# Performance work log

Measured on AMD Instinct MI355X. Metric: run time of the kernel, lower is better.

## Reference

```python
import jax, jax.numpy as jnp
import numpy as np

N_SETS = [5, 5, 5, 5, 5]
N_SAMPLES = 16384


def _rule_indices(n_sets):
    # (R, n) grid of all fuzzy-set index combinations, same as torch.meshgrid(indexing='ij')
    grids = np.meshgrid(*[np.arange(s) for s in n_sets], indexing='ij')
    return np.stack([g.reshape(-1) for g in grids], axis=1)  # (R, n)


def setup_inputs() -> dict:
    key = jax.random.key(0)
    ks = jax.random.split(key, len(N_SETS))
    return {
        f"m{j}": jax.random.uniform(ks[j], (N_SAMPLES, N_SETS[j]), dtype=jnp.float32)
        for j in range(len(N_SETS))
    }


def reference(m0, m1, m2, m3, m4):
    memberships = [m0, m1, m2, m3, m4]
    ri = jnp.asarray(_rule_indices(N_SETS))  # (R, n) static rule-index table
    # Gather per-variable membership columns for every rule and AND (prod) across variables.
    # Equivalent to padding/stacking + gather + prod over the variable axis in the original,
    # but avoids materializing the (n, N, R) int index tensor.
    ant = memberships[0][:, ri[:, 0]]  # (N, R)
    for j in range(1, len(N_SETS)):
        ant = ant * memberships[j][:, ri[:, j]]
    return ant  # (N, R)
```

## Files before the change

kernel.cpp:

```cpp
#include <hip/hip_runtime.h>


#define NSAMP 16384
#define NRULE 3125

__global__ __launch_bounds__(256) void antecedents_kernel(
    const float* __restrict__ m0, const float* __restrict__ m1,
    const float* __restrict__ m2, const float* __restrict__ m3,
    const float* __restrict__ m4, float* __restrict__ out)
{
    __shared__ float p012[125];
    __shared__ float p34[25];

    const int i = blockIdx.x;
    const unsigned t = threadIdx.x;

    if (t < 125u) {
        const unsigned a = t / 25u;
        const unsigned b = (t / 5u) % 5u;
        const unsigned c = t % 5u;
        p012[t] = m0[i * 5 + a] * m1[i * 5 + b] * m2[i * 5 + c];
    } else if (t < 150u) {
        const unsigned u = t - 125u;
        const unsigned d = u / 5u;
        const unsigned e = u % 5u;
        p34[u] = m3[i * 5 + d] * m4[i * 5 + e];
    }
    __syncthreads();

    float* __restrict__ orow = out + (size_t)i * NRULE;
    for (unsigned r = t; r < NRULE; r += 256u) {
        const unsigned hi = r / 25u;
        const unsigned lo = r - hi * 25u;
        orow[r] = p012[hi] * p34[lo];
    }
}

extern "C" void kernel_launch(void* const* d_in, const int* in_sizes, int n_in,
                              void* d_out, int out_size, void* d_ws, size_t ws_size,
                              hipStream_t stream) {
    const float* m0 = (const float*)d_in[0];
    const float* m1 = (const float*)d_in[1];
    const float* m2 = (const float*)d_in[2];
    const float* m3 = (const float*)d_in[3];
    const float* m4 = (const float*)d_in[4];
    float* out = (float*)d_out;

    antecedents_kernel<<<NSAMP, 256, 0, stream>>>(m0, m1, m2, m3, m4, out);
}
```

Before: 38.08 us.

## Process eight rows per block and write output with float4 stores

Each block now handles eight sample rows, building their partial-product tables together in shared memory. It writes the contiguous eight-row output chunk with 16-byte vector stores. This is meant to cut per-block launch and sync overhead and to use wider, fully aligned stores, since eight rows of 3125 floats is a multiple of four. The cost is more index arithmetic per element, including divisions by NRULE and 25, and fewer blocks in the grid.

Result: slower. 39.45 us (+3.6%).

```diff
diff --git a/kernel.cpp b/kernel.cpp
--- a/kernel.cpp
+++ b/kernel.cpp
@@ -3,36 +3,54 @@
 
 #define NSAMP 16384
 #define NRULE 3125
+#define ROWS_PER_BLOCK 8
+#define CHUNK_ELEMS (ROWS_PER_BLOCK * NRULE)
+#define CHUNK_VEC4 (CHUNK_ELEMS / 4)
 
 __global__ __launch_bounds__(256) void antecedents_kernel(
     const float* __restrict__ m0, const float* __restrict__ m1,
     const float* __restrict__ m2, const float* __restrict__ m3,
     const float* __restrict__ m4, float* __restrict__ out)
 {
-    __shared__ float p012[125];
-    __shared__ float p34[25];
+    __shared__ float p012[ROWS_PER_BLOCK][125];
+    __shared__ float p34[ROWS_PER_BLOCK][25];
 
-    const int i = blockIdx.x;
     const unsigned t = threadIdx.x;
+    const unsigned row0 = blockIdx.x * ROWS_PER_BLOCK;
 
-    if (t < 125u) {
-        const unsigned a = t / 25u;
-        const unsigned b = (t / 5u) % 5u;
-        const unsigned c = t % 5u;
-        p012[t] = m0[i * 5 + a] * m1[i * 5 + b] * m2[i * 5 + c];
-    } else if (t < 150u) {
-        const unsigned u = t - 125u;
-        const unsigned d = u / 5u;
-        const unsigned e = u % 5u;
-        p34[u] = m3[i * 5 + d] * m4[i * 5 + e];
+    for (unsigned u = t; u < ROWS_PER_BLOCK * 150u; u += 256u) {
+        const unsigned rr = u / 150u;
+        const unsigned k = u - rr * 150u;
+        const unsigned row = row0 + rr;
+        if (k < 125u) {
+            const unsigned a = k / 25u;
+            const unsigned b = (k / 5u) % 5u;
+            const unsigned c = k % 5u;
+            p012[rr][k] = m0[row * 5 + a] * m1[row * 5 + b] * m2[row * 5 + c];
+        } else {
+            const unsigned kk = k - 125u;
+            p34[rr][kk] = m3[row * 5 + kk / 5u] * m4[row * 5 + kk % 5u];
+        }
     }
     __syncthreads();
 
-    float* __restrict__ orow = out + (size_t)i * NRULE;
-    for (unsigned r = t; r < NRULE; r += 256u) {
-        const unsigned hi = r / 25u;
-        const unsigned lo = r - hi * 25u;
-        orow[r] = p012[hi] * p34[lo];
+    float4* __restrict__ outv =
+        (float4*)(out + (size_t)blockIdx.x * CHUNK_ELEMS);
+
+    for (unsigned q = t; q < CHUNK_VEC4; q += 256u) {
+        float4 v;
+        unsigned fe = q * 4u;
+        float* vp = (float*)&v;
+#pragma unroll
+        for (int k = 0; k < 4; ++k) {
+            const unsigned rr = fe / (unsigned)NRULE;
+            const unsigned r = fe - rr * (unsigned)NRULE;
+            const unsigned hi = r / 25u;
+            const unsigned lo = r - hi * 25u;
+            vp[k] = p012[rr][hi] * p34[rr][lo];
+            ++fe;
+        }
+        outv[q] = v;
     }
 }
 
@@ -46,5 +64,6 @@
     const float* m4 = (const float*)d_in[4];
     float* out = (float*)d_out;
 
-    antecedents_kernel<<<NSAMP, 256, 0, stream>>>(m0, m1, m2, m3, m4, out);
+    antecedents_kernel<<<NSAMP / ROWS_PER_BLOCK, 256, 0, stream>>>(
+        m0, m1, m2, m3, m4, out);
 }
```
